# Kernel tuning notes

Hardware: AMD Instinct MI355X
Metric: run time of the kernel (lower is better)

## Reference

```python
import jax, jax.numpy as jnp
import numpy as np

N, M, K = 2048, 128, 8
LAMBDA_BELIEF = 1.0
LAMBDA_MODEL = 1.0


def _spd(key, n, k, scale=0.3):
    # well-conditioned SPD covariance: A A^T + I
    a = jax.random.normal(key, (n, k, k)) * scale
    return a @ jnp.swapaxes(a, -1, -2) + jnp.eye(k, dtype=jnp.float32)


def _frame(key, n, k, scale=0.1):
    # invertible near-identity gauge frame Omega
    return jnp.eye(k, dtype=jnp.float32) + scale * jax.random.normal(key, (n, k, k))


def setup_inputs() -> dict:
    key = jax.random.key(0)
    ks = jax.random.split(key, 13)
    return {
        'W': jax.random.uniform(ks[0], (N, M)),
        'mu_p': jax.random.normal(ks[1], (N, K)),
        'sigma_p': _spd(ks[2], N, K),
        'mu_q_parent': jax.random.normal(ks[3], (M, K)),
        'sigma_q_parent': _spd(ks[4], M, K),
        'omega_child': _frame(ks[5], N, K),
        'omega_parent': _frame(ks[6], M, K),
        'mu_r': jax.random.normal(ks[7], (N, K)),
        'sigma_r': _spd(ks[8], N, K),
        'mu_s_parent': jax.random.normal(ks[9], (M, K)),
        'sigma_s_parent': _spd(ks[10], M, K),
        'omega_m_child': _frame(ks[11], N, K),
        'omega_m_parent': _frame(ks[12], M, K),
    }


def gaussian_kl(mu0, s0, mu1, s1):
    """KL(N(mu0,s0) || N(mu1,s1)); broadcasts over leading dims."""
    k = mu0.shape[-1]
    s1_inv_s0 = jnp.linalg.solve(s1, jnp.broadcast_to(s0, s1.shape))
    tr = jnp.trace(s1_inv_s0, axis1=-2, axis2=-1)
    diff = mu1 - mu0
    sol = jnp.linalg.solve(s1, diff[..., None])[..., 0]
    maha = jnp.sum(diff * sol, axis=-1)
    ld1 = jnp.linalg.slogdet(s1)[1]
    ld0 = jnp.linalg.slogdet(s0)[1]
    return 0.5 * (tr + maha - k + ld1 - ld0)


def _topdown(W, mu_child, sigma_child, mu_parent, sigma_parent, om_child, om_parent):
    # transport_{i,alpha} = Omega_i @ Omega_alpha^{-1}  -> (N, M, K, K)
    om_parent_inv = jnp.linalg.inv(om_parent)
    T = jnp.einsum('nab,mbc->nmac', om_child, om_parent_inv)
    mu_t = jnp.einsum('nmab,mb->nma', T, mu_parent)                 # (N, M, K)
    sigma_t = jnp.einsum('nmab,mbc,nmdc->nmad', T, sigma_parent, T)  # (N, M, K, K)
    kl = gaussian_kl(mu_child[:, None], sigma_child[:, None], mu_t, sigma_t)  # (N, M)
    return jnp.sum(W * kl)


def reference(W, mu_p, sigma_p, mu_q_parent, sigma_q_parent, omega_child, omega_parent,
              mu_r, sigma_r, mu_s_parent, sigma_s_parent, omega_m_child, omega_m_parent):
    belief_topdown = _topdown(W, mu_p, sigma_p, mu_q_parent, sigma_q_parent,
                              omega_child, omega_parent)
    model_topdown = _topdown(W, mu_r, sigma_r, mu_s_parent, sigma_s_parent,
                             omega_m_child, omega_m_parent)
    total = LAMBDA_BELIEF * belief_topdown + LAMBDA_MODEL * model_topdown
    return (total, belief_topdown, model_topdown)
```

## Files before the change

kernel.cpp:

```cpp
#include <hip/hip_runtime.h>


#define N_TOT 2048
#define M_TOT 128
#define NC 8
#define MC 16
#define MCH (M_TOT / MC)
#define NCH (N_TOT / NC)
#define NBLOCKS (2 * NC * MC)
#define GLEN 48

__device__ __forceinline__ void load64(float* dst, const float* __restrict__ src) {
    const float4* p4 = (const float4*)src;
#pragma unroll
    for (int q = 0; q < 16; ++q) {
        float4 v = p4[q];
        dst[4*q+0] = v.x; dst[4*q+1] = v.y; dst[4*q+2] = v.z; dst[4*q+3] = v.w;
    }
}

__global__ __launch_bounds__(256, 1)
void he_main(const float* __restrict__ W,
             const float* __restrict__ mu_p,  const float* __restrict__ sig_p,
             const float* __restrict__ mu_qp, const float* __restrict__ sig_qp,
             const float* __restrict__ om_c,  const float* __restrict__ om_p,
             const float* __restrict__ mu_r,  const float* __restrict__ sig_r,
             const float* __restrict__ mu_sp, const float* __restrict__ sig_sp,
             const float* __restrict__ om_mc, const float* __restrict__ om_mp,
             double* __restrict__ partials)
{
    __shared__ float g_l[MCH][GLEN];
    __shared__ double red[4];

    const int b   = blockIdx.x;
    const int td  = b >> 7;
    const int nc  = (b >> 4) & 7;
    const int mc  = b & 15;
    const int tid = threadIdx.x;

    const float* muC = td ? mu_r   : mu_p;
    const float* SC  = td ? sig_r  : sig_p;
    const float* OC  = td ? om_mc  : om_c;
    const float* muP = td ? mu_sp  : mu_qp;
    const float* SP  = td ? sig_sp : sig_qp;
    const float* OP  = td ? om_mp  : om_p;

    if (tid < MCH) {
        const int m = mc * MCH + tid;

        float L[64];
        load64(L, SP + m * 64);
        float invd[8];
        float lsp = 0.f;
#pragma unroll
        for (int i = 0; i < 8; ++i) {
#pragma unroll
            for (int j = 0; j <= i; ++j) {
                float s = L[i*8+j];
#pragma unroll
                for (int k = 0; k < j; ++k) s -= L[i*8+k] * L[j*8+k];
                if (j == i) {
                    float d = sqrtf(s);
                    L[i*8+i] = d; invd[i] = 1.0f / d; lsp += logf(d);
                } else {
                    L[i*8+j] = s * invd[j];
                }
            }
        }
        lsp *= 2.0f;

        float z[8]; float cq = 0.f;
#pragma unroll
        for (int i = 0; i < 8; ++i) {
            float s = muP[m*8 + i];
#pragma unroll
            for (int k = 0; k < i; ++k) s -= L[i*8+k] * z[k];
            z[i] = s * invd[i];
            cq += z[i] * z[i];
        }

        float B[64];
        load64(B, OP + m * 64);
        float Y[64];
#pragma unroll
        for (int i = 0; i < 8; ++i) {
#pragma unroll
            for (int c8 = 0; c8 < 8; ++c8) {
                float s = B[i*8+c8];
#pragma unroll
                for (int k = 0; k < i; ++k) s -= L[i*8+k] * Y[k*8+c8];
                Y[i*8+c8] = s * invd[i];
            }
        }

        int t = 0;
#pragma unroll
        for (int a = 0; a < 8; ++a) {
#pragma unroll
            for (int bb = a; bb < 8; ++bb) {
                float s = 0.f;
#pragma unroll
                for (int i = 0; i < 8; ++i) s += Y[i*8+a] * Y[i*8+bb];
                g_l[tid][t++] = (bb == a) ? s : 2.0f * s;
            }
        }
#pragma unroll
        for (int a = 0; a < 8; ++a) {
            float s = 0.f;
#pragma unroll
            for (int i = 0; i < 8; ++i) s += Y[i*8+a] * z[i];
            g_l[tid][36 + a] = -2.0f * s;
        }

        float lb = 0.f;
#pragma unroll
        for (int k = 0; k < 8; ++k) {
            lb += logf(fabsf(B[k*8+k]));
            float r = 1.0f / B[k*8+k];
#pragma unroll
            for (int i = k + 1; i < 8; ++i) {
                float f = B[i*8+k] * r;
#pragma unroll
                for (int j = k + 1; j < 8; ++j) B[i*8+j] -= f * B[k*8+j];
            }
        }
        g_l[tid][44] = cq - 2.0f * lb + lsp;
        g_l[tid][45] = 0.f; g_l[tid][46] = 0.f; g_l[tid][47] = 0.f;
    }

    const int n = nc * NCH + tid;

    float wreg[MCH];
    float wsum = 0.f;
    {
        const float4* wrow = (const float4*)(W + n * M_TOT + mc * MCH);
#pragma unroll
        for (int q = 0; q < MCH / 4; ++q) {
            float4 v = wrow[q];
            wreg[4*q+0] = v.x; wreg[4*q+1] = v.y; wreg[4*q+2] = v.z; wreg[4*q+3] = v.w;
            wsum += v.x + v.y + v.z + v.w;
        }
    }

    float Um[64];
    load64(Um, OC + n * 64);
    float la = 0.f; float invu[8];
#pragma unroll
    for (int k = 0; k < 8; ++k) {
        la += logf(fabsf(Um[k*8+k]));
        float r = 1.0f / Um[k*8+k];
        invu[k] = r;
#pragma unroll
        for (int i = k + 1; i < 8; ++i) {
            float f = Um[i*8+k] * r;
            Um[i*8+k] = f;
#pragma unroll
            for (int j = k + 1; j < 8; ++j) Um[i*8+j] -= f * Um[k*8+j];
        }
    }

    float Ls[64];
    load64(Ls, SC + n * 64);
    float invd2[8];
    float ls0 = 0.f;
#pragma unroll
    for (int i = 0; i < 8; ++i) {
#pragma unroll
        for (int j = 0; j <= i; ++j) {
            float s = Ls[i*8+j];
#pragma unroll
            for (int k = 0; k < j; ++k) s -= Ls[i*8+k] * Ls[j*8+k];
            if (j == i) {
                float d = sqrtf(s);
                Ls[i*8+i] = d; invd2[i] = 1.0f / d; ls0 += logf(d);
            } else {
                Ls[i*8+j] = s * invd2[j];
            }
        }
    }
    ls0 *= 2.0f;

    float Mt[64];
#pragma unroll
    for (int j = 0; j < 8; ++j) {
        float y[8];
#pragma unroll
        for (int i = 0; i < 8; ++i) {
            if (i < j) { y[i] = 0.f; }
            else {
                float s = Ls[i*8+j];
#pragma unroll
                for (int k = j; k < i; ++k) s -= Um[i*8+k] * y[k];
                y[i] = s;
            }
        }
#pragma unroll
        for (int i = 7; i >= 0; --i) {
            float s = y[i];
#pragma unroll
            for (int k = i + 1; k < 8; ++k) s -= Um[i*8+k] * Mt[k*8+j];
            Mt[i*8+j] = s * invu[i];
        }
    }

    float mu0[8];
    {
        const float4* p4 = (const float4*)(muC + n * 8);
        float4 v0 = p4[0], v1 = p4[1];
        mu0[0]=v0.x; mu0[1]=v0.y; mu0[2]=v0.z; mu0[3]=v0.w;
        mu0[4]=v1.x; mu0[5]=v1.y; mu0[6]=v1.z; mu0[7]=v1.w;
    }
    float u[8];
    {
        float y[8];
#pragma unroll
        for (int i = 0; i < 8; ++i) {
            float s = mu0[i];
#pragma unroll
            for (int k = 0; k < i; ++k) s -= Um[i*8+k] * y[k];
            y[i] = s;
        }
#pragma unroll
        for (int i = 7; i >= 0; --i) {
            float s = y[i];
#pragma unroll
            for (int k = i + 1; k < 8; ++k) s -= Um[i*8+k] * u[k];
            u[i] = s * invu[i];
        }
    }

    float dv[GLEN];
    {
        int t = 0;
#pragma unroll
        for (int a = 0; a < 8; ++a) {
#pragma unroll
            for (int bb = a; bb < 8; ++bb) {
                float s = u[a] * u[bb];
#pragma unroll
                for (int k = 0; k < 8; ++k) s += Mt[a*8+k] * Mt[bb*8+k];
                dv[t++] = s;
            }
        }
    }
#pragma unroll
    for (int a = 0; a < 8; ++a) dv[36 + a] = u[a];
    dv[44] = 1.0f; dv[45] = 0.f; dv[46] = 0.f; dv[47] = 0.f;

    const float tn = 2.0f * la - ls0;

    __syncthreads();

    float acc = 0.f;
#pragma unroll
    for (int j = 0; j < MCH; ++j) {
        const float4* gr = (const float4*)&g_l[j][0];
        float dot = 0.f;
#pragma unroll
        for (int q = 0; q < GLEN / 4; ++q) {
            float4 gv = gr[q];
            dot += gv.x * dv[4*q+0] + gv.y * dv[4*q+1]
                 + gv.z * dv[4*q+2] + gv.w * dv[4*q+3];
        }
        acc += wreg[j] * dot;
    }

    double part = 0.5 * ((double)acc + (double)wsum * ((double)tn - 8.0));

#pragma unroll
    for (int off = 32; off > 0; off >>= 1) part += __shfl_down(part, off, 64);
    if ((tid & 63) == 0) red[tid >> 6] = part;
    __syncthreads();
    if (tid == 0) partials[b] = red[0] + red[1] + red[2] + red[3];
}

__global__ void he_finalize(const double* __restrict__ partials, float* __restrict__ out)
{
    __shared__ double sh[4];
    const int tid = threadIdx.x;
    double v = partials[tid];
#pragma unroll
    for (int off = 32; off > 0; off >>= 1) v += __shfl_down(v, off, 64);
    if ((tid & 63) == 0) sh[tid >> 6] = v;
    __syncthreads();
    if (tid == 0) {
        double belief = sh[0] + sh[1];
        double model  = sh[2] + sh[3];
        out[0] = (float)(belief + model);
        out[1] = (float)belief;
        out[2] = (float)model;
    }
}

extern "C" void kernel_launch(void* const* d_in, const int* in_sizes, int n_in,
                              void* d_out, int out_size, void* d_ws, size_t ws_size,
                              hipStream_t stream)
{
    const float* W      = (const float*)d_in[0];
    const float* mu_p   = (const float*)d_in[1];
    const float* sig_p  = (const float*)d_in[2];
    const float* mu_qp  = (const float*)d_in[3];
    const float* sig_qp = (const float*)d_in[4];
    const float* om_c   = (const float*)d_in[5];
    const float* om_p   = (const float*)d_in[6];
    const float* mu_r   = (const float*)d_in[7];
    const float* sig_r  = (const float*)d_in[8];
    const float* mu_sp  = (const float*)d_in[9];
    const float* sig_sp = (const float*)d_in[10];
    const float* om_mc  = (const float*)d_in[11];
    const float* om_mp  = (const float*)d_in[12];

    double* partials = (double*)d_ws;

    he_main<<<NBLOCKS, 256, 0, stream>>>(W, mu_p, sig_p, mu_qp, sig_qp, om_c, om_p,
                                         mu_r, sig_r, mu_sp, sig_sp, om_mc, om_mp,
                                         partials);
    he_finalize<<<1, 256, 0, stream>>>(partials, (float*)d_out);
}
```

Measured before the change: 92.71 us.

## Double M-chunk grid, raise occupancy, use fast intrinsics and log-of-products

Doubles the number of M chunks so the grid has 512 blocks with 4 parents per block, and raises launch_bounds to 2 blocks per SM. It replaces sqrt, reciprocal and log with fast AMDGCN intrinsics and computes a single log of a product of diagonals instead of summing logs. It also reuses register arrays in place to cut register pressure, and widens the finalize kernel to 512 threads. The cost is that each block recomputes its per-child factorization over a smaller M range, so the redundant per-n work doubles, and the fast math lowers precision.

```diff
diff --git a/kernel.cpp b/kernel.cpp
--- a/kernel.cpp
+++ b/kernel.cpp
@@ -4,12 +4,18 @@
 #define N_TOT 2048
 #define M_TOT 128
 #define NC 8
-#define MC 16
+#define MC 32
 #define MCH (M_TOT / MC)
 #define NCH (N_TOT / NC)
 #define NBLOCKS (2 * NC * MC)
 #define GLEN 48
 
+#define LN2F 0.69314718055994531f
+
+__device__ __forceinline__ float frcp(float x)  { return __builtin_amdgcn_rcpf(x); }
+__device__ __forceinline__ float fsqrt(float x) { return __builtin_amdgcn_sqrtf(x); }
+__device__ __forceinline__ float flogabs(float x) { return LN2F * __log2f(fabsf(x)); }
+
 __device__ __forceinline__ void load64(float* dst, const float* __restrict__ src) {
     const float4* p4 = (const float4*)src;
 #pragma unroll
@@ -19,7 +25,7 @@
     }
 }
 
-__global__ __launch_bounds__(256, 1)
+__global__ __launch_bounds__(256, 2)
 void he_main(const float* __restrict__ W,
              const float* __restrict__ mu_p,  const float* __restrict__ sig_p,
              const float* __restrict__ mu_qp, const float* __restrict__ sig_qp,
@@ -33,9 +39,9 @@
     __shared__ double red[4];
 
     const int b   = blockIdx.x;
-    const int td  = b >> 7;
-    const int nc  = (b >> 4) & 7;
-    const int mc  = b & 15;
+    const int td  = b >> 8;
+    const int nc  = (b >> 5) & 7;
+    const int mc  = b & 31;
     const int tid = threadIdx.x;
 
     const float* muC = td ? mu_r   : mu_p;
@@ -51,7 +57,6 @@
         float L[64];
         load64(L, SP + m * 64);
         float invd[8];
-        float lsp = 0.f;
 #pragma unroll
         for (int i = 0; i < 8; ++i) {
 #pragma unroll
@@ -60,14 +65,13 @@
 #pragma unroll
                 for (int k = 0; k < j; ++k) s -= L[i*8+k] * L[j*8+k];
                 if (j == i) {
-                    float d = sqrtf(s);
-                    L[i*8+i] = d; invd[i] = 1.0f / d; lsp += logf(d);
+                    float d = fsqrt(s);
+                    L[i*8+i] = d; invd[i] = frcp(d);
                 } else {
                     L[i*8+j] = s * invd[j];
                 }
             }
         }
-        lsp *= 2.0f;
 
         float z[8]; float cq = 0.f;
 #pragma unroll
@@ -79,17 +83,16 @@
             cq += z[i] * z[i];
         }
 
-        float B[64];
-        load64(B, OP + m * 64);
-        float Y[64];
+        float Yb[64];
+        load64(Yb, OP + m * 64);
 #pragma unroll
         for (int i = 0; i < 8; ++i) {
 #pragma unroll
             for (int c8 = 0; c8 < 8; ++c8) {
-                float s = B[i*8+c8];
-#pragma unroll
-                for (int k = 0; k < i; ++k) s -= L[i*8+k] * Y[k*8+c8];
-                Y[i*8+c8] = s * invd[i];
+                float s = Yb[i*8+c8];
+#pragma unroll
+                for (int k = 0; k < i; ++k) s -= L[i*8+k] * Yb[k*8+c8];
+                Yb[i*8+c8] = s * invd[i];
             }
         }
 
@@ -100,7 +103,7 @@
             for (int bb = a; bb < 8; ++bb) {
                 float s = 0.f;
 #pragma unroll
-                for (int i = 0; i < 8; ++i) s += Y[i*8+a] * Y[i*8+bb];
+                for (int i = 0; i < 8; ++i) s += Yb[i*8+a] * Yb[i*8+bb];
                 g_l[tid][t++] = (bb == a) ? s : 2.0f * s;
             }
         }
@@ -108,47 +111,43 @@
         for (int a = 0; a < 8; ++a) {
             float s = 0.f;
 #pragma unroll
-            for (int i = 0; i < 8; ++i) s += Y[i*8+a] * z[i];
+            for (int i = 0; i < 8; ++i) s += Yb[i*8+a] * z[i];
             g_l[tid][36 + a] = -2.0f * s;
         }
 
-        float lb = 0.f;
+        float prodY = 1.f;
 #pragma unroll
         for (int k = 0; k < 8; ++k) {
-            lb += logf(fabsf(B[k*8+k]));
-            float r = 1.0f / B[k*8+k];
+            prodY *= Yb[k*8+k];
+            float r = frcp(Yb[k*8+k]);
 #pragma unroll
             for (int i = k + 1; i < 8; ++i) {
-                float f = B[i*8+k] * r;
-#pragma unroll
-                for (int j = k + 1; j < 8; ++j) B[i*8+j] -= f * B[k*8+j];
-            }
-        }
-        g_l[tid][44] = cq - 2.0f * lb + lsp;
+                float f = Yb[i*8+k] * r;
+#pragma unroll
+                for (int j = k + 1; j < 8; ++j) Yb[i*8+j] -= f * Yb[k*8+j];
+            }
+        }
+        g_l[tid][44] = cq - 2.0f * flogabs(prodY);
         g_l[tid][45] = 0.f; g_l[tid][46] = 0.f; g_l[tid][47] = 0.f;
     }
 
     const int n = nc * NCH + tid;
 
     float wreg[MCH];
-    float wsum = 0.f;
+    float wsum;
     {
-        const float4* wrow = (const float4*)(W + n * M_TOT + mc * MCH);
-#pragma unroll
-        for (int q = 0; q < MCH / 4; ++q) {
-            float4 v = wrow[q];
-            wreg[4*q+0] = v.x; wreg[4*q+1] = v.y; wreg[4*q+2] = v.z; wreg[4*q+3] = v.w;
-            wsum += v.x + v.y + v.z + v.w;
-        }
+        float4 v = *(const float4*)(W + n * M_TOT + mc * MCH);
+        wreg[0] = v.x; wreg[1] = v.y; wreg[2] = v.z; wreg[3] = v.w;
+        wsum = v.x + v.y + v.z + v.w;
     }
 
     float Um[64];
     load64(Um, OC + n * 64);
-    float la = 0.f; float invu[8];
+    float prodUA = 1.f; float invu[8];
 #pragma unroll
     for (int k = 0; k < 8; ++k) {
-        la += logf(fabsf(Um[k*8+k]));
-        float r = 1.0f / Um[k*8+k];
+        prodUA *= Um[k*8+k];
+        float r = frcp(Um[k*8+k]);
         invu[k] = r;
 #pragma unroll
         for (int i = k + 1; i < 8; ++i) {
@@ -162,7 +161,7 @@
     float Ls[64];
     load64(Ls, SC + n * 64);
     float invd2[8];
-    float ls0 = 0.f;
+    float prodLs = 1.f;
 #pragma unroll
     for (int i = 0; i < 8; ++i) {
 #pragma unroll
@@ -171,47 +170,42 @@
 #pragma unroll
             for (int k = 0; k < j; ++k) s -= Ls[i*8+k] * Ls[j*8+k];
             if (j == i) {
-                float d = sqrtf(s);
-                Ls[i*8+i] = d; invd2[i] = 1.0f / d; ls0 += logf(d);
+                float d = fsqrt(s);
+                Ls[i*8+i] = d; prodLs *= d; invd2[i] = frcp(d);
             } else {
                 Ls[i*8+j] = s * invd2[j];
             }
         }
     }
-    ls0 *= 2.0f;
-
-    float Mt[64];
+
+    const float tn = 2.0f * flogabs(prodUA * frcp(prodLs));
+
 #pragma unroll
     for (int j = 0; j < 8; ++j) {
         float y[8];
 #pragma unroll
-        for (int i = 0; i < 8; ++i) {
-            if (i < j) { y[i] = 0.f; }
-            else {
-                float s = Ls[i*8+j];
-#pragma unroll
-                for (int k = j; k < i; ++k) s -= Um[i*8+k] * y[k];
-                y[i] = s;
-            }
+        for (int i = j; i < 8; ++i) {
+            float s = Ls[i*8+j];
+#pragma unroll
+            for (int k = j; k < i; ++k) s -= Um[i*8+k] * y[k];
+            y[i] = s;
         }
 #pragma unroll
         for (int i = 7; i >= 0; --i) {
-            float s = y[i];
-#pragma unroll
-            for (int k = i + 1; k < 8; ++k) s -= Um[i*8+k] * Mt[k*8+j];
-            Mt[i*8+j] = s * invu[i];
-        }
-    }
-
-    float mu0[8];
+            float s = (i >= j) ? y[i] : 0.f;
+#pragma unroll
+            for (int k = i + 1; k < 8; ++k) s -= Um[i*8+k] * Ls[k*8+j];
+            Ls[i*8+j] = s * invu[i];
+        }
+    }
+
+    float u[8];
     {
+        float mu0[8];
         const float4* p4 = (const float4*)(muC + n * 8);
         float4 v0 = p4[0], v1 = p4[1];
         mu0[0]=v0.x; mu0[1]=v0.y; mu0[2]=v0.z; mu0[3]=v0.w;
         mu0[4]=v1.x; mu0[5]=v1.y; mu0[6]=v1.z; mu0[7]=v1.w;
-    }
-    float u[8];
-    {
         float y[8];
 #pragma unroll
         for (int i = 0; i < 8; ++i) {
@@ -238,7 +232,7 @@
             for (int bb = a; bb < 8; ++bb) {
                 float s = u[a] * u[bb];
 #pragma unroll
-                for (int k = 0; k < 8; ++k) s += Mt[a*8+k] * Mt[bb*8+k];
+                for (int k = 0; k < 8; ++k) s += Ls[a*8+k] * Ls[bb*8+k];
                 dv[t++] = s;
             }
         }
@@ -246,8 +240,6 @@
 #pragma unroll
     for (int a = 0; a < 8; ++a) dv[36 + a] = u[a];
     dv[44] = 1.0f; dv[45] = 0.f; dv[46] = 0.f; dv[47] = 0.f;
-
-    const float tn = 2.0f * la - ls0;
 
     __syncthreads();
 
@@ -276,7 +268,7 @@
 
 __global__ void he_finalize(const double* __restrict__ partials, float* __restrict__ out)
 {
-    __shared__ double sh[4];
+    __shared__ double sh[8];
     const int tid = threadIdx.x;
     double v = partials[tid];
 #pragma unroll
@@ -284,8 +276,8 @@
     if ((tid & 63) == 0) sh[tid >> 6] = v;
     __syncthreads();
     if (tid == 0) {
-        double belief = sh[0] + sh[1];
-        double model  = sh[2] + sh[3];
+        double belief = sh[0] + sh[1] + sh[2] + sh[3];
+        double model  = sh[4] + sh[5] + sh[6] + sh[7];
         out[0] = (float)(belief + model);
         out[1] = (float)belief;
         out[2] = (float)model;
@@ -315,5 +307,5 @@
     he_main<<<NBLOCKS, 256, 0, stream>>>(W, mu_p, sig_p, mu_qp, sig_qp, om_c, om_p,
                                          mu_r, sig_r, mu_sp, sig_sp, om_mc, om_mp,
                                          partials);
-    he_finalize<<<1, 256, 0, stream>>>(partials, (float*)d_out);
+    he_finalize<<<1, 512, 0, stream>>>(partials, (float*)d_out);
 }
```

After: 92.91 us. No clear change (+0.2%).
